# Kernel optimization log

Hardware: AMD Instinct MI355X
Metric: run time of the kernel (lower is better)

Reference implementation:

```python
import jax, jax.numpy as jnp
import numpy as np

SELECT_SIZE = 64
SM_SCALE = 0.07216878364870322  # 192 ** -0.5
V_HEAD_DIM = 128


def setup_inputs() -> dict:
    key = jax.random.key(0)
    k1, k2, k3, k4 = jax.random.split(key, 4)
    B, S, Hq, G, TOPK = 4, 2048, 16, 4, 16
    T = B * S
    NB = S // SELECT_SIZE  # 32 blocks per sequence
    q = jax.random.normal(k1, (T, Hq, 192), dtype=jnp.float32)
    k = jax.random.normal(k2, (T, Hq, 192), dtype=jnp.float32)
    v = jax.random.normal(k3, (T, Hq, V_HEAD_DIM), dtype=jnp.float32)
    idx = jax.random.randint(k4, (T, G, TOPK), 0, NB, dtype=jnp.int32)
    # guarantee block 0 is always selected so every causal row has >=1 valid key
    idx = idx.at[..., 0].set(0)
    idx = jnp.sort(idx, axis=-1)
    return {"q": q, "k": k, "v": v, "selected_indices": idx,
            "batch_size": B, "seq_len": S}


def reference(q, k, v, selected_indices, batch_size, seq_len):
    B, S = batch_size, seq_len
    Hq = q.shape[1]
    G = selected_indices.shape[1]
    Hg = Hq // G  # query heads per selection-score group
    nb = (S + SELECT_SIZE - 1) // SELECT_SIZE
    dv = v.shape[-1]

    # un-ragged: B equal-length sequences
    qg = q.reshape(B, S, G, Hg, -1)
    kg = k.reshape(B, S, G, Hg, -1)
    vg = v.reshape(B, S, G, Hg, -1)
    idx = selected_indices.reshape(B, S, G, -1)

    # which KV blocks are selected for each (query position, group): [B,S,G,nb]
    allowed_blk = (idx[..., None] == jnp.arange(nb, dtype=idx.dtype)).any(axis=-2)
    blk_of_pos = jnp.arange(S) // SELECT_SIZE
    pos_ok = allowed_blk[..., blk_of_pos]  # [B, Tq, G, Skv]
    causal = jnp.arange(S)[:, None] >= jnp.arange(S)[None, :]
    mask = pos_ok & causal[None, :, None, :]          # [B, Tq, G, Skv]
    mask = mask.transpose(0, 2, 1, 3)[:, :, None]      # [B, G, 1, Tq, Skv]

    scores = jnp.einsum('btghd,bsghd->bghts', qg, kg) * SM_SCALE
    scores = jnp.where(mask, scores, jnp.float32(-1e30))
    attn = jax.nn.softmax(scores, axis=-1)
    o = jnp.einsum('bghts,bsghd->btghd', attn, vg)
    return o.reshape(B * S, Hq * dv)
```

## Files before the change

### kernel.cpp

```cpp
#include <hip/hip_runtime.h>


typedef __attribute__((ext_vector_type(8))) _Float16 half8;
typedef __attribute__((ext_vector_type(4))) _Float16 half4;
typedef __attribute__((ext_vector_type(4))) float f32x4;
typedef __attribute__((ext_vector_type(4))) unsigned int u32x4;

__device__ __forceinline__ half8 cvt8s(const float4* p, float s) {
  float4 a = p[0], b = p[1];
  half8 r;
  r[0] = (_Float16)(a.x * s); r[1] = (_Float16)(a.y * s);
  r[2] = (_Float16)(a.z * s); r[3] = (_Float16)(a.w * s);
  r[4] = (_Float16)(b.x * s); r[5] = (_Float16)(b.y * s);
  r[6] = (_Float16)(b.z * s); r[7] = (_Float16)(b.w * s);
  return r;
}

__device__ __forceinline__ void async16(const void* g, void* l) {
  __builtin_amdgcn_global_load_lds(
      (const __attribute__((address_space(1))) void*)g,
      (__attribute__((address_space(3))) void*)l, 16, 0, 0);
}

__device__ __forceinline__ f32x4 vmax4(f32x4 a, f32x4 b) {
  f32x4 r;
  r[0] = fmaxf(a[0], b[0]); r[1] = fmaxf(a[1], b[1]);
  r[2] = fmaxf(a[2], b[2]); r[3] = fmaxf(a[3], b[3]);
  return r;
}

__global__ __launch_bounds__(256) void kv_prep(const float* __restrict__ k,
                                               const float* __restrict__ v,
                                               _Float16* __restrict__ kf,
                                               _Float16* __restrict__ vf) {
  __shared__ __align__(16) _Float16 kbuf[64 * 200];
  __shared__ __align__(16) _Float16 vbuf[64 * 136];
  int blk = blockIdx.x;
  int bh = blk >> 5, kb = blk & 31;
  int b = bh >> 4, h = bh & 15;
  int tid = threadIdx.x;

  const float* ksrc = k + ((long)(b * 2048 + kb * 64) * 16 + h) * 192;
  const float* vsrc = v + ((long)(b * 2048 + kb * 64) * 16 + h) * 128;

#pragma unroll
  for (int it = 0; it < 12; ++it) {
    int idx = it * 256 + tid;
    int kk = idx / 48, c4 = idx - kk * 48;
    float4 x = *(const float4*)(ksrc + (long)kk * 3072 + c4 * 4);
    int s = ((kk >> 2) & 3) * 16 + ((kk >> 4) << 2) + (kk & 3);
    half4 hx = {(_Float16)x.x, (_Float16)x.y, (_Float16)x.z, (_Float16)x.w};
    *(half4*)(&kbuf[s * 200 + c4 * 4]) = hx;
  }
#pragma unroll
  for (int it = 0; it < 8; ++it) {
    int idx = it * 256 + tid;
    int kk = idx >> 5, c4 = idx & 31;
    float4 x = *(const float4*)(vsrc + (long)kk * 2048 + c4 * 4);
    half4 hx = {(_Float16)x.x, (_Float16)x.y, (_Float16)x.z, (_Float16)x.w};
    *(half4*)(&vbuf[kk * 136 + c4 * 4]) = hx;
  }
  __syncthreads();

  _Float16* kdst = kf + (long)blk * 12288;
#pragma unroll
  for (int it = 0; it < 6; ++it) {
    int oct = it * 256 + tid;
    int frag = oct >> 6, lane = oct & 63;
    int ntile = frag / 6, kc = frag - ntile * 6;
    int s = ntile * 16 + (lane & 15);
    int d = kc * 32 + ((lane >> 4) << 3);
    *(half8*)(kdst + (long)oct * 8) = *(const half8*)(&kbuf[s * 200 + d]);
  }

  _Float16* vdst = vf + (long)blk * 8192;
#pragma unroll
  for (int it = 0; it < 4; ++it) {
    int oct = it * 256 + tid;
    int frag = oct >> 6, lane = oct & 63;
    int n0 = frag >> 1, kc = frag & 1;
    int dv = n0 * 16 + (lane & 15);
    int kbase = kc * 32 + ((lane >> 4) << 3);
    half8 o;
#pragma unroll
    for (int j = 0; j < 8; ++j) o[j] = vbuf[(kbase + j) * 136 + dv];
    *(half8*)(vdst + (long)oct * 8) = o;
  }
}

__global__ __launch_bounds__(512) void attn_main(const float* __restrict__ q,
                                                 const int* __restrict__ idx,
                                                 const _Float16* __restrict__ kf,
                                                 const _Float16* __restrict__ vf,
                                                 float* __restrict__ out) {
  constexpr float SCL = 0.07216878364870322f * 1.4426950408889634f;
  int id = (int)blockIdx.x;
  int u = 15 - (id >> 6);
  int bh = id & 63;
  int h = bh & 15, b = bh >> 4, g = h >> 2;
  int qlo = 2 * u, qhi = 2 * u + 1;
  int tid = threadIdx.x;
  int w = tid >> 6, L = tid & 63;
  int Lm = L & 15, Lq = L >> 4;
  int tile = w >> 2;
  int m0 = (w & 3) * 16;
  int myqb = qlo + tile;
  int t0 = b * 2048 + qlo * 64;
  long trow = t0 + tile * 64 + m0 + Lm;

  __shared__ __align__(16) char sh_kv[40960];
  __shared__ __align__(16) _Float16 Pbuf[8][16 * 72];
  __shared__ unsigned un_sh[8];
  char* lk = sh_kv;
  char* lv = sh_kv + 24576;

  half8 qa[6];
  const float* qrow = q + (trow * 16 + h) * 192;
#pragma unroll
  for (int c = 0; c < 6; ++c) qa[c] = cvt8s((const float4*)(qrow + c * 32 + Lq * 8), SCL);

  unsigned mrow = 0;
  {
    const int4* ip = (const int4*)(idx + (trow * 4 + g) * 16);
#pragma unroll
    for (int e = 0; e < 4; ++e) {
      int4 iv = ip[e];
      mrow |= (1u << iv.x) | (1u << iv.y) | (1u << iv.z) | (1u << iv.w);
    }
  }
  unsigned un = mrow;
#pragma unroll
  for (int o = 32; o; o >>= 1) un |= __shfl_xor(un, o, 64);
  if (L == 0) un_sh[w] = un;
  __syncthreads();
  unsigned bm = un_sh[0] | un_sh[1] | un_sh[2] | un_sh[3] |
                un_sh[4] | un_sh[5] | un_sh[6] | un_sh[7];
  unsigned bmask = bm & ((2u << qhi) - 1);

  f32x4 Oacc[8];
#pragma unroll
  for (int n0 = 0; n0 < 8; ++n0) Oacc[n0] = (f32x4){0.f, 0.f, 0.f, 0.f};
  float m_i = -1e30f, l_i = 0.f;

  const char* kfb = (const char*)(kf + (long)((b * 16 + h) * 32) * 12288);
  const char* vfb = (const char*)(vf + (long)((b * 16 + h) * 32) * 8192);
  _Float16* pw = &Pbuf[w][0];
  const half8* lkf = (const half8*)lk;
  const half8* lvf = (const half8*)lv;

  auto stage = [&](int kb) {
    const char* kg = kfb + (long)kb * 24576;
    const char* vg = vfb + (long)kb * 16384;
#pragma unroll
    for (int c = 0; c < 3; ++c) {
      int ch = w + c * 8;
      async16(kg + ch * 1024 + L * 16, lk + ch * 1024);
    }
#pragma unroll
    for (int c = 0; c < 2; ++c) {
      int ch = w + c * 8;
      async16(vg + ch * 1024 + L * 16, lv + ch * 1024);
    }
  };

  auto compute = [&](int kb, bool lastb) __attribute__((always_inline)) {
    f32x4 S[4];
    __builtin_amdgcn_s_setprio(1);
#pragma unroll
    for (int nt = 0; nt < 4; ++nt) {
      f32x4 acc = {0.f, 0.f, 0.f, 0.f};
#pragma unroll
      for (int c = 0; c < 6; ++c)
        acc = __builtin_amdgcn_mfma_f32_16x16x32_f16(lkf[(nt * 6 + c) * 64 + L], qa[c], acc, 0, 0, 0);
      S[nt] = acc;
    }
    __builtin_amdgcn_s_setprio(0);

    float p[4][4];
    float msel = ((mrow >> kb) & 1u) ? 1.0f : 0.0f;
    if (!lastb) {
      f32x4 t = vmax4(vmax4(S[0], S[1]), vmax4(S[2], S[3]));
      float rmax = fmaxf(fmaxf(t[0], t[1]), fmaxf(t[2], t[3]));
      rmax = fmaxf(rmax, __shfl_xor(rmax, 16));
      rmax = fmaxf(rmax, __shfl_xor(rmax, 32));
      if (__any(rmax > m_i + 8.0f)) {
        float mn = fmaxf(m_i, rmax);
        float av = __builtin_amdgcn_exp2f(m_i - mn);
        m_i = mn;
        l_i *= av;
#pragma unroll
        for (int n0 = 0; n0 < 8; ++n0) Oacc[n0] *= av;
      }
      float ps[4];
#pragma unroll
      for (int nt = 0; nt < 4; ++nt) {
        float s0 = 0.f, s1 = 0.f;
#pragma unroll
        for (int i = 0; i < 4; i += 2) {
          float a = __builtin_amdgcn_exp2f(S[nt][i] - m_i) * msel;
          float c = __builtin_amdgcn_exp2f(S[nt][i + 1] - m_i) * msel;
          p[nt][i] = a; p[nt][i + 1] = c;
          s0 += a; s1 += c;
        }
        ps[nt] = s0 + s1;
      }
      float psum = (ps[0] + ps[1]) + (ps[2] + ps[3]);
      psum += __shfl_xor(psum, 16);
      psum += __shfl_xor(psum, 32);
      l_i += psum;
    } else {
      float sc[4][4];
      float rmax = -1e30f;
#pragma unroll
      for (int nt = 0; nt < 4; ++nt)
#pragma unroll
        for (int i = 0; i < 4; ++i) {
          int key = Lq * 16 + nt * 4 + i;
          bool ok = (msel != 0.f) && (key <= m0 + Lm);
          float v = ok ? S[nt][i] : -1e30f;
          sc[nt][i] = v;
          rmax = fmaxf(rmax, v);
        }
      rmax = fmaxf(rmax, __shfl_xor(rmax, 16));
      rmax = fmaxf(rmax, __shfl_xor(rmax, 32));
      float mn = fmaxf(m_i, rmax);
      float av = __builtin_amdgcn_exp2f(m_i - mn);
      m_i = mn;
      float ps[4];
#pragma unroll
      for (int nt = 0; nt < 4; ++nt) {
        float s0 = 0.f;
#pragma unroll
        for (int i = 0; i < 4; ++i) {
          float a = __builtin_amdgcn_exp2f(sc[nt][i] - mn);
          p[nt][i] = a;
          s0 += a;
        }
        ps[nt] = s0;
      }
      float psum = (ps[0] + ps[1]) + (ps[2] + ps[3]);
      psum += __shfl_xor(psum, 16);
      psum += __shfl_xor(psum, 32);
      l_i = l_i * av + psum;
#pragma unroll
      for (int n0 = 0; n0 < 8; ++n0) Oacc[n0] *= av;
    }

    asm volatile("s_waitcnt lgkmcnt(0)" ::: "memory");
    u32x4 w0, w1;
    {
      auto c00 = __builtin_amdgcn_cvt_pkrtz(p[0][0], p[0][1]);
      auto c01 = __builtin_amdgcn_cvt_pkrtz(p[0][2], p[0][3]);
      auto c10 = __builtin_amdgcn_cvt_pkrtz(p[1][0], p[1][1]);
      auto c11 = __builtin_amdgcn_cvt_pkrtz(p[1][2], p[1][3]);
      auto c20 = __builtin_amdgcn_cvt_pkrtz(p[2][0], p[2][1]);
      auto c21 = __builtin_amdgcn_cvt_pkrtz(p[2][2], p[2][3]);
      auto c30 = __builtin_amdgcn_cvt_pkrtz(p[3][0], p[3][1]);
      auto c31 = __builtin_amdgcn_cvt_pkrtz(p[3][2], p[3][3]);
      w0[0] = __builtin_bit_cast(unsigned, c00); w0[1] = __builtin_bit_cast(unsigned, c01);
      w0[2] = __builtin_bit_cast(unsigned, c10); w0[3] = __builtin_bit_cast(unsigned, c11);
      w1[0] = __builtin_bit_cast(unsigned, c20); w1[1] = __builtin_bit_cast(unsigned, c21);
      w1[2] = __builtin_bit_cast(unsigned, c30); w1[3] = __builtin_bit_cast(unsigned, c31);
    }
    *(u32x4*)(pw + Lm * 72 + Lq * 16) = w0;
    *(u32x4*)(pw + Lm * 72 + Lq * 16 + 8) = w1;
    asm volatile("s_waitcnt lgkmcnt(0)" ::: "memory");

    __builtin_amdgcn_s_setprio(1);
#pragma unroll
    for (int kc = 0; kc < 2; ++kc) {
      half8 pfr = *(const half8*)(pw + Lm * 72 + kc * 32 + Lq * 8);
#pragma unroll
      for (int n0 = 0; n0 < 8; ++n0)
        Oacc[n0] = __builtin_amdgcn_mfma_f32_16x16x32_f16(lvf[(n0 * 2 + kc) * 64 + L], pfr, Oacc[n0], 0, 0, 0);
    }
    __builtin_amdgcn_s_setprio(0);
  };

  unsigned rem = bmask;
  while (rem) {
    int kb = (int)__builtin_ctz(rem);
    rem &= rem - 1;
    stage(kb);
    asm volatile("s_waitcnt vmcnt(0)" ::: "memory");
    __syncthreads();
    if (kb <= myqb && ((un >> kb) & 1u)) compute(kb, kb == myqb);
    __syncthreads();
  }

  float inv = 1.f / l_i;
  float* orow = out + trow * 2048 + h * 128 + Lq * 4;
#pragma unroll
  for (int n0 = 0; n0 < 8; ++n0) {
    f32x4 o = Oacc[n0] * inv;
    *(f32x4*)(orow + n0 * 16) = o;
  }
}

extern "C" void kernel_launch(void* const* d_in, const int* in_sizes, int n_in,
                              void* d_out, int out_size, void* d_ws, size_t ws_size,
                              hipStream_t stream) {
  const float* q = (const float*)d_in[0];
  const float* k = (const float*)d_in[1];
  const float* v = (const float*)d_in[2];
  const int* idx = (const int*)d_in[3];
  _Float16* kf = (_Float16*)d_ws;
  _Float16* vf = kf + (size_t)2048 * 12288;
  float* out = (float*)d_out;
  kv_prep<<<2048, 256, 0, stream>>>(k, v, kf, vf);
  attn_main<<<1024, 512, 0, stream>>>(q, idx, kf, vf, out);
}
```

Measured before the change: 381.2 us.

## Double-buffer K tiles, prefetch V via registers, and pass P through shuffles

Replaces the single-buffered stage-wait-compute loop with a software pipeline. The next selected block's K tile is loaded asynchronously into a second LDS buffer and its V tile into registers while the current block is computed. The V registers are written to LDS after a barrier. The P matrix handoff between the two MFMA stages now uses cross-lane shuffles instead of an LDS round trip. The block-mask reduction now uses wave shuffles instead of shared memory and a barrier. The loop always starts at block 0 and drops the lowest mask bit on the first pass, so it relies on block 0 always being selected, which the test inputs guarantee. It also adds register pressure and one more LDS buffer.

```diff
diff --git a/kernel.cpp b/kernel.cpp
--- a/kernel.cpp
+++ b/kernel.cpp
@@ -108,33 +108,36 @@
   int t0 = b * 2048 + qlo * 64;
   long trow = t0 + tile * 64 + m0 + Lm;
 
-  __shared__ __align__(16) char sh_kv[40960];
-  __shared__ __align__(16) _Float16 Pbuf[8][16 * 72];
-  __shared__ unsigned un_sh[8];
-  char* lk = sh_kv;
-  char* lv = sh_kv + 24576;
+  __shared__ __align__(16) char sh_k[2][24576];
+  __shared__ __align__(16) char sh_v[16384];
 
   half8 qa[6];
   const float* qrow = q + (trow * 16 + h) * 192;
 #pragma unroll
   for (int c = 0; c < 6; ++c) qa[c] = cvt8s((const float4*)(qrow + c * 32 + Lq * 8), SCL);
 
-  unsigned mrow = 0;
+  unsigned rm0 = 0, rm1 = 0;
   {
-    const int4* ip = (const int4*)(idx + (trow * 4 + g) * 16);
+    const int4* ip0 = (const int4*)(idx + ((long)(t0 + L) * 4 + g) * 16);
+    const int4* ip1 = (const int4*)(idx + ((long)(t0 + 64 + L) * 4 + g) * 16);
 #pragma unroll
     for (int e = 0; e < 4; ++e) {
-      int4 iv = ip[e];
-      mrow |= (1u << iv.x) | (1u << iv.y) | (1u << iv.z) | (1u << iv.w);
-    }
-  }
-  unsigned un = mrow;
-#pragma unroll
-  for (int o = 32; o; o >>= 1) un |= __shfl_xor(un, o, 64);
-  if (L == 0) un_sh[w] = un;
-  __syncthreads();
-  unsigned bm = un_sh[0] | un_sh[1] | un_sh[2] | un_sh[3] |
-                un_sh[4] | un_sh[5] | un_sh[6] | un_sh[7];
+      int4 i0 = ip0[e], i1 = ip1[e];
+      rm0 |= (1u << i0.x) | (1u << i0.y) | (1u << i0.z) | (1u << i0.w);
+      rm1 |= (1u << i1.x) | (1u << i1.y) | (1u << i1.z) | (1u << i1.w);
+    }
+  }
+  unsigned bm = rm0 | rm1;
+#pragma unroll
+  for (int o = 1; o < 64; o <<= 1) bm |= __shfl_xor(bm, o, 64);
+  unsigned rmT = tile ? rm1 : rm0;
+  unsigned g16 = rmT;
+  g16 |= __shfl_xor(g16, 1);
+  g16 |= __shfl_xor(g16, 2);
+  g16 |= __shfl_xor(g16, 4);
+  g16 |= __shfl_xor(g16, 8);
+  unsigned un = __shfl(g16, m0, 64);
+  unsigned mrow = __shfl(rmT, m0 + Lm, 64);
   unsigned bmask = bm & ((2u << qhi) - 1);
 
   f32x4 Oacc[8];
@@ -144,26 +147,31 @@
 
   const char* kfb = (const char*)(kf + (long)((b * 16 + h) * 32) * 12288);
   const char* vfb = (const char*)(vf + (long)((b * 16 + h) * 32) * 8192);
-  _Float16* pw = &Pbuf[w][0];
-  const half8* lkf = (const half8*)lk;
-  const half8* lvf = (const half8*)lv;
-
-  auto stage = [&](int kb) {
-    const char* kg = kfb + (long)kb * 24576;
-    const char* vg = vfb + (long)kb * 16384;
+
+  auto stageK = [&](int kb2, char* dst) {
+    const char* kg = kfb + (long)kb2 * 24576;
 #pragma unroll
     for (int c = 0; c < 3; ++c) {
       int ch = w + c * 8;
-      async16(kg + ch * 1024 + L * 16, lk + ch * 1024);
-    }
-#pragma unroll
-    for (int c = 0; c < 2; ++c) {
-      int ch = w + c * 8;
-      async16(vg + ch * 1024 + L * 16, lv + ch * 1024);
+      async16(kg + ch * 1024 + L * 16, dst + ch * 1024);
     }
   };
-
-  auto compute = [&](int kb, bool lastb) __attribute__((always_inline)) {
+  u32x4 vreg[2];
+  auto loadVreg = [&](int kb2) {
+    const char* vg = vfb + (long)kb2 * 16384;
+#pragma unroll
+    for (int c = 0; c < 2; ++c)
+      vreg[c] = *(const u32x4*)(vg + (w + c * 8) * 1024 + L * 16);
+  };
+  auto writeV = [&]() {
+#pragma unroll
+    for (int c = 0; c < 2; ++c)
+      *(u32x4*)(sh_v + (w + c * 8) * 1024 + L * 16) = vreg[c];
+  };
+
+  const half8* lvf = (const half8*)sh_v;
+
+  auto compute = [&](int kb, bool lastb, const half8* lkf) __attribute__((always_inline)) {
     f32x4 S[4];
     __builtin_amdgcn_s_setprio(1);
 #pragma unroll
@@ -246,46 +254,60 @@
       for (int n0 = 0; n0 < 8; ++n0) Oacc[n0] *= av;
     }
 
-    asm volatile("s_waitcnt lgkmcnt(0)" ::: "memory");
-    u32x4 w0, w1;
-    {
-      auto c00 = __builtin_amdgcn_cvt_pkrtz(p[0][0], p[0][1]);
-      auto c01 = __builtin_amdgcn_cvt_pkrtz(p[0][2], p[0][3]);
-      auto c10 = __builtin_amdgcn_cvt_pkrtz(p[1][0], p[1][1]);
-      auto c11 = __builtin_amdgcn_cvt_pkrtz(p[1][2], p[1][3]);
-      auto c20 = __builtin_amdgcn_cvt_pkrtz(p[2][0], p[2][1]);
-      auto c21 = __builtin_amdgcn_cvt_pkrtz(p[2][2], p[2][3]);
-      auto c30 = __builtin_amdgcn_cvt_pkrtz(p[3][0], p[3][1]);
-      auto c31 = __builtin_amdgcn_cvt_pkrtz(p[3][2], p[3][3]);
-      w0[0] = __builtin_bit_cast(unsigned, c00); w0[1] = __builtin_bit_cast(unsigned, c01);
-      w0[2] = __builtin_bit_cast(unsigned, c10); w0[3] = __builtin_bit_cast(unsigned, c11);
-      w1[0] = __builtin_bit_cast(unsigned, c20); w1[1] = __builtin_bit_cast(unsigned, c21);
-      w1[2] = __builtin_bit_cast(unsigned, c30); w1[3] = __builtin_bit_cast(unsigned, c31);
-    }
-    *(u32x4*)(pw + Lm * 72 + Lq * 16) = w0;
-    *(u32x4*)(pw + Lm * 72 + Lq * 16 + 8) = w1;
-    asm volatile("s_waitcnt lgkmcnt(0)" ::: "memory");
+    unsigned w8[8];
+#pragma unroll
+    for (int nt = 0; nt < 4; ++nt) {
+      w8[2 * nt]     = __builtin_bit_cast(unsigned, __builtin_amdgcn_cvt_pkrtz(p[nt][0], p[nt][1]));
+      w8[2 * nt + 1] = __builtin_bit_cast(unsigned, __builtin_amdgcn_cvt_pkrtz(p[nt][2], p[nt][3]));
+    }
+    half8 pfr[2];
+#pragma unroll
+    for (int kc = 0; kc < 2; ++kc) {
+      int src = ((Lq >> 1) + 2 * kc) * 16 + Lm;
+      u32x4 d;
+#pragma unroll
+      for (int e = 0; e < 4; ++e) {
+        unsigned lo = (unsigned)__shfl((int)w8[e], src, 64);
+        unsigned hi = (unsigned)__shfl((int)w8[e + 4], src, 64);
+        d[e] = (Lq & 1) ? hi : lo;
+      }
+      pfr[kc] = __builtin_bit_cast(half8, d);
+    }
 
     __builtin_amdgcn_s_setprio(1);
 #pragma unroll
-    for (int kc = 0; kc < 2; ++kc) {
-      half8 pfr = *(const half8*)(pw + Lm * 72 + kc * 32 + Lq * 8);
+    for (int kc = 0; kc < 2; ++kc)
 #pragma unroll
       for (int n0 = 0; n0 < 8; ++n0)
-        Oacc[n0] = __builtin_amdgcn_mfma_f32_16x16x32_f16(lvf[(n0 * 2 + kc) * 64 + L], pfr, Oacc[n0], 0, 0, 0);
-    }
+        Oacc[n0] = __builtin_amdgcn_mfma_f32_16x16x32_f16(lvf[(n0 * 2 + kc) * 64 + L], pfr[kc], Oacc[n0], 0, 0, 0);
     __builtin_amdgcn_s_setprio(0);
   };
 
+  stageK(0, sh_k[0]);
+  loadVreg(0);
+  __syncthreads();
+  writeV();
+  __syncthreads();
+
   unsigned rem = bmask;
-  while (rem) {
-    int kb = (int)__builtin_ctz(rem);
+  int kb = 0, cur = 0;
+  for (;;) {
     rem &= rem - 1;
-    stage(kb);
-    asm volatile("s_waitcnt vmcnt(0)" ::: "memory");
+    int nxt = rem ? (int)__builtin_ctz(rem) : -1;
+    if (nxt >= 0) {
+      stageK(nxt, sh_k[cur ^ 1]);
+      loadVreg(nxt);
+    }
+
+    if (kb <= myqb && ((un >> kb) & 1u))
+      compute(kb, kb == myqb, (const half8*)sh_k[cur]);
+
     __syncthreads();
-    if (kb <= myqb && ((un >> kb) & 1u)) compute(kb, kb == myqb);
+    if (nxt < 0) break;
+    writeV();
     __syncthreads();
+    cur ^= 1;
+    kb = nxt;
   }
 
   float inv = 1.f / l_i;
```

Result: slower. 393.8 us (+3.3%).
